# Optimization experiments

Measured on AMD Instinct MI355X. Metric: run time of the kernel, lower is better.

## Reference

```python
import jax, jax.numpy as jnp
import numpy as np

NUM_PATCHES = 4
PATCH_RADIUS = 0.2


def setup_inputs() -> dict:
    key = jax.random.key(0)
    points = jax.random.normal(key, (64, 65536, 6), dtype=jnp.float32)
    return {"points": points}


def _fps(xyz, n_samples):
    """Furthest point sampling (pointnet2 convention: start at index 0).
    xyz: (B, N, 3) -> (B, n_samples) int32 indices."""
    B, N, _ = xyz.shape

    def body(carry, _):
        min_d, last_idx = carry                                   # (B,N), (B,)
        last = jnp.take_along_axis(xyz, last_idx[:, None, None], axis=1)  # (B,1,3)
        d = jnp.sum((xyz - last) ** 2, axis=-1)                   # (B,N)
        min_d = jnp.minimum(min_d, d)
        nxt = jnp.argmax(min_d, axis=1).astype(jnp.int32)
        return (min_d, nxt), last_idx

    init = (jnp.full((B, N), 1e10, dtype=xyz.dtype),
            jnp.zeros((B,), dtype=jnp.int32))
    (_, _), idxs = jax.lax.scan(body, init, None, length=n_samples)
    return idxs.T                                                  # (B, n_samples)


def reference(points):
    B, N, C = points.shape
    xyz = points[..., :3]

    # 1) pick patch centers via FPS
    centers_idx = _fps(xyz, NUM_PATCHES)                           # (B,P)
    centers = jnp.take_along_axis(xyz, centers_idx[..., None], axis=1)  # (B,P,3)

    # 2) distance of every point to nearest center -> drop mask
    dist = jnp.linalg.norm(xyz[:, :, None, :] - centers[:, None, :, :], axis=-1)  # (B,N,P)
    min_dist = jnp.min(dist, axis=2)                               # (B,N)
    keep = min_dist >= PATCH_RADIUS                                # (B,N) bool, True = kept

    # 3) stable compaction: kept points first (original order preserved),
    #    then repeat-fill pattern valid_points[j % num_valid]
    order = jnp.argsort(jnp.logical_not(keep).astype(jnp.int32), axis=1, stable=True)  # (B,N)
    num_valid = jnp.sum(keep, axis=1)                              # (B,)
    j = jnp.arange(N, dtype=jnp.int32)[None, :]                    # (1,N)
    k = j % jnp.maximum(num_valid, 1)[:, None]                     # (B,N)
    src = jnp.take_along_axis(order, k, axis=1)                    # (B,N)
    out = jnp.take_along_axis(points, src[..., None], axis=1)      # (B,N,C)

    # all points dropped -> zeros (matches torch branch)
    return jnp.where((num_valid > 0)[:, None, None], out, jnp.zeros_like(out))
```

## Files before the change

kernel.cpp:

```cpp
#include <hip/hip_runtime.h>
#include <stdint.h>

#define NN 65536
#define BB 64
#define TPB 256
#define BLKS_PER_B 16
#define GRID (BB * BLKS_PER_B)
#define PPB 4096
#define LPT 16

__device__ __forceinline__ float sqdist(float x, float y, float z,
                                        float cx, float cy, float cz) {
    float dx = __fsub_rn(x, cx);
    float dy = __fsub_rn(y, cy);
    float dz = __fsub_rn(z, cz);
    return __fadd_rn(__fadd_rn(__fmul_rn(dx, dx), __fmul_rn(dy, dy)),
                     __fmul_rn(dz, dz));
}

__device__ __forceinline__ unsigned long long pack_key(float v, int i) {
    return ((unsigned long long)__float_as_uint(v) << 32) |
           (unsigned long long)(0xFFFFFFFFu - (unsigned)i);
}

template<int NC>
__global__ __launch_bounds__(TPB) void fps_pass(
        const float* __restrict__ pts, unsigned long long* best) {
    const int gb = blockIdx.x;
    const int b = gb >> 4, blk = gb & 15;
    const int tid = threadIdx.x;
    const int lane = tid & 63, wid = tid >> 6;
    const float* base = pts + (size_t)b * NN * 6;

    float cx[NC], cy[NC], cz[NC];
    cx[0] = base[0]; cy[0] = base[1]; cz[0] = base[2];
    #pragma unroll
    for (int k = 1; k < NC; ++k) {
        unsigned long long key = best[(k - 1) * BB + b];
        int idx = (int)(0xFFFFFFFFu - (unsigned)(key & 0xFFFFFFFFu));
        const float* p = base + (size_t)idx * 6;
        cx[k] = p[0]; cy[k] = p[1]; cz[k] = p[2];
    }

    float bestv = -1.0f; int besti = 0x7fffffff;
    #pragma unroll
    for (int l = 0; l < LPT; ++l) {
        const int p = blk * PPB + l * TPB + tid;
        const float* q = base + (size_t)p * 6;
        float2 xy = *(const float2*)q;
        float  zz = q[2];
        float d = sqdist(xy.x, xy.y, zz, cx[0], cy[0], cz[0]);
        #pragma unroll
        for (int k = 1; k < NC; ++k)
            d = fminf(d, sqdist(xy.x, xy.y, zz, cx[k], cy[k], cz[k]));
        if (d > bestv) { bestv = d; besti = p; }
    }
    unsigned long long key = pack_key(bestv, besti);
    #pragma unroll
    for (int off = 32; off > 0; off >>= 1) {
        unsigned long long ok = __shfl_down(key, off, 64);
        if (ok > key) key = ok;
    }
    __shared__ unsigned long long s_k[4];
    if (lane == 0) s_k[wid] = key;
    __syncthreads();
    if (tid == 0) {
        unsigned long long bk = s_k[0];
        #pragma unroll
        for (int w = 1; w < 4; ++w) bk = (s_k[w] > bk) ? s_k[w] : bk;
        atomicMax(&best[(NC - 1) * BB + b], bk);
    }
}

__global__ __launch_bounds__(TPB) void fps_final(
        const float* __restrict__ pts, const unsigned long long* __restrict__ best,
        uint64_t* __restrict__ masks) {
    const int gb = blockIdx.x;
    const int b = gb >> 4, blk = gb & 15;
    const int tid = threadIdx.x;
    const int lane = tid & 63, wid = tid >> 6;
    const float* base = pts + (size_t)b * NN * 6;

    float cx[4], cy[4], cz[4];
    cx[0] = base[0]; cy[0] = base[1]; cz[0] = base[2];
    #pragma unroll
    for (int k = 1; k < 4; ++k) {
        unsigned long long key = best[(k - 1) * BB + b];
        int idx = (int)(0xFFFFFFFFu - (unsigned)(key & 0xFFFFFFFFu));
        const float* p = base + (size_t)idx * 6;
        cx[k] = p[0]; cy[k] = p[1]; cz[k] = p[2];
    }
    uint64_t* mb = masks + (size_t)b * 1024;

    #pragma unroll
    for (int l = 0; l < LPT; ++l) {
        const int p = blk * PPB + l * TPB + tid;
        const float* q = base + (size_t)p * 6;
        float2 xy = *(const float2*)q;
        float  zz = q[2];
        float d = sqdist(xy.x, xy.y, zz, cx[0], cy[0], cz[0]);
        #pragma unroll
        for (int k = 1; k < 4; ++k)
            d = fminf(d, sqdist(xy.x, xy.y, zz, cx[k], cy[k], cz[k]));
        int keep = (__fsqrt_rn(d) >= 0.2f) ? 1 : 0;
        uint64_t m = __ballot(keep);
        if (lane == 0) mb[blk * 64 + l * 4 + wid] = m;
    }
}

__global__ __launch_bounds__(TPB) void compact_kernel(
        const uint64_t* __restrict__ masks, int* __restrict__ valid,
        int* __restrict__ numvalid) {
    const int b = blockIdx.x;
    const int tid = threadIdx.x;
    const int lane = tid & 63, wid = tid >> 6;
    const uint64_t* mb = masks + (size_t)b * 1024;
    uint64_t w0 = mb[tid * 4 + 0], w1 = mb[tid * 4 + 1];
    uint64_t w2 = mb[tid * 4 + 2], w3 = mb[tid * 4 + 3];
    int cnt4 = __popcll(w0) + __popcll(w1) + __popcll(w2) + __popcll(w3);
    int incl = cnt4;
    #pragma unroll
    for (int off = 1; off < 64; off <<= 1) {
        int v = __shfl_up(incl, off, 64);
        if (lane >= off) incl += v;
    }
    __shared__ int s_ws[4], s_wo[4];
    if (lane == 63) s_ws[wid] = incl;
    __syncthreads();
    if (tid == 0) {
        int run = 0;
        #pragma unroll
        for (int w = 0; w < 4; ++w) { s_wo[w] = run; run += s_ws[w]; }
        numvalid[b] = run;
    }
    __syncthreads();
    int pos = s_wo[wid] + incl - cnt4;
    int* vb = valid + ((size_t)b << 16);
    const int pbase = tid * 256;
    uint64_t ws[4] = { w0, w1, w2, w3 };
    #pragma unroll
    for (int wdx = 0; wdx < 4; ++wdx) {
        uint64_t m = ws[wdx];
        int pb = pbase + wdx * 64;
        while (m) {
            int k = __builtin_ctzll(m);
            m &= m - 1;
            vb[pos++] = pb + k;
        }
    }
}

__global__ __launch_bounds__(256) void gather_kernel(
        const float* __restrict__ pts, const int* __restrict__ valid,
        const int* __restrict__ numvalid, float* __restrict__ out) {
    const int idx = blockIdx.x * 256 + threadIdx.x;
    const int b = idx >> 16;
    const int j = idx & (NN - 1);
    const int nv = numvalid[b];
    float2* o = (float2*)(out + (size_t)idx * 6);
    if (nv <= 0) {
        float2 z = make_float2(0.f, 0.f);
        o[0] = z; o[1] = z; o[2] = z;
        return;
    }
    unsigned jj = (unsigned)j % (unsigned)nv;
    int src = valid[((size_t)b << 16) + jj];
    const float2* p = (const float2*)(pts + ((size_t)(b << 16) + (size_t)src) * 6);
    o[0] = p[0]; o[1] = p[1]; o[2] = p[2];
}

extern "C" void kernel_launch(void* const* d_in, const int* in_sizes, int n_in,
                              void* d_out, int out_size, void* d_ws, size_t ws_size,
                              hipStream_t stream) {
    const float* pts = (const float*)d_in[0];
    float* out = (float*)d_out;

    unsigned long long* best = (unsigned long long*)d_ws;
    int*      numvalid = (int*)((char*)d_ws + (4 << 10));
    uint64_t* masks    = (uint64_t*)((char*)d_ws + (64 << 10));
    int*      valid    = (int*)((char*)d_ws + (1 << 20));

    hipMemsetAsync(best, 0, 3 * BB * sizeof(unsigned long long), stream);

    fps_pass<1><<<GRID, TPB, 0, stream>>>(pts, best);
    fps_pass<2><<<GRID, TPB, 0, stream>>>(pts, best);
    fps_pass<3><<<GRID, TPB, 0, stream>>>(pts, best);
    fps_final<<<GRID, TPB, 0, stream>>>(pts, best, masks);
    compact_kernel<<<BB, TPB, 0, stream>>>(masks, valid, numvalid);
    gather_kernel<<<(BB * NN) / 256, 256, 0, stream>>>(pts, valid, numvalid, out);
}
```

Baseline: 278.3 us.

## Fuse compaction into gather and replace atomics with per-block partial keys

Removes the separate compaction kernel and its index array by having each gather block rebuild the per-batch prefix of mask popcounts in shared memory. Each output point then finds its source with a binary search plus an in-word select. The FPS passes now write per-block partial max keys, which each consumer reduces, replacing the memset and atomicMax. The FPS grid doubles to 32 blocks per batch with fewer points per thread. The cost is redundant prefix work in every gather block and a 32-way key reduction repeated per block.

```diff
diff --git a/kernel.cpp b/kernel.cpp
--- a/kernel.cpp
+++ b/kernel.cpp
@@ -4,10 +4,15 @@
 #define NN 65536
 #define BB 64
 #define TPB 256
-#define BLKS_PER_B 16
-#define GRID (BB * BLKS_PER_B)
-#define PPB 4096
-#define LPT 16
+
+#define FBPB 32
+#define FGRID (BB * FBPB)
+#define FPPB 2048
+#define FLPT 8
+
+#define GBPB 16
+#define GGRID (BB * GBPB)
+#define GLPT 16
 
 __device__ __forceinline__ float sqdist(float x, float y, float z,
                                         float cx, float cy, float cz) {
@@ -23,150 +28,192 @@
            (unsigned long long)(0xFFFFFFFFu - (unsigned)i);
 }
 
+__device__ __forceinline__ int key_idx(unsigned long long key) {
+    return (int)(0xFFFFFFFFu - (unsigned)(key & 0xFFFFFFFFu));
+}
+
+__device__ __forceinline__ int reduce_part(const unsigned long long* partKey,
+                                           int a, int b) {
+    const unsigned long long* s = partKey + a * FGRID + b * FBPB;
+    unsigned long long bk = s[0];
+    #pragma unroll
+    for (int w = 1; w < FBPB; ++w) bk = (s[w] > bk) ? s[w] : bk;
+    return key_idx(bk);
+}
+
 template<int NC>
 __global__ __launch_bounds__(TPB) void fps_pass(
-        const float* __restrict__ pts, unsigned long long* best) {
+        const float* __restrict__ pts, unsigned long long* partKey) {
+    const int gb = blockIdx.x;
+    const int b = gb >> 5, blk = gb & 31;
+    const int tid = threadIdx.x;
+    const int lane = tid & 63, wid = tid >> 6;
+    const float* base = pts + (size_t)b * NN * 6;
+
+    float cx[NC], cy[NC], cz[NC];
+    cx[0] = base[0]; cy[0] = base[1]; cz[0] = base[2];
+    #pragma unroll
+    for (int k = 1; k < NC; ++k) {
+        int idx = reduce_part(partKey, k - 1, b);
+        const float* p = base + (size_t)idx * 6;
+        cx[k] = p[0]; cy[k] = p[1]; cz[k] = p[2];
+    }
+
+    float bestv = -1.0f; int besti = 0x7fffffff;
+    #pragma unroll
+    for (int l = 0; l < FLPT; ++l) {
+        const int p = blk * FPPB + l * TPB + tid;
+        const float* q = base + (size_t)p * 6;
+        float2 xy = *(const float2*)q;
+        float  zz = q[2];
+        float d = sqdist(xy.x, xy.y, zz, cx[0], cy[0], cz[0]);
+        #pragma unroll
+        for (int k = 1; k < NC; ++k)
+            d = fminf(d, sqdist(xy.x, xy.y, zz, cx[k], cy[k], cz[k]));
+        if (d > bestv) { bestv = d; besti = p; }
+    }
+    unsigned long long key = pack_key(bestv, besti);
+    #pragma unroll
+    for (int off = 32; off > 0; off >>= 1) {
+        unsigned long long ok = __shfl_down(key, off, 64);
+        if (ok > key) key = ok;
+    }
+    __shared__ unsigned long long s_k[4];
+    if (lane == 0) s_k[wid] = key;
+    __syncthreads();
+    if (tid == 0) {
+        unsigned long long bk = s_k[0];
+        #pragma unroll
+        for (int w = 1; w < 4; ++w) bk = (s_k[w] > bk) ? s_k[w] : bk;
+        partKey[(NC - 1) * FGRID + gb] = bk;
+    }
+}
+
+__global__ __launch_bounds__(TPB) void fps_final(
+        const float* __restrict__ pts,
+        const unsigned long long* __restrict__ partKey,
+        uint64_t* __restrict__ masks) {
+    const int gb = blockIdx.x;
+    const int b = gb >> 5, blk = gb & 31;
+    const int tid = threadIdx.x;
+    const int lane = tid & 63, wid = tid >> 6;
+    const float* base = pts + (size_t)b * NN * 6;
+
+    float cx[4], cy[4], cz[4];
+    cx[0] = base[0]; cy[0] = base[1]; cz[0] = base[2];
+    #pragma unroll
+    for (int k = 1; k < 4; ++k) {
+        int idx = reduce_part(partKey, k - 1, b);
+        const float* p = base + (size_t)idx * 6;
+        cx[k] = p[0]; cy[k] = p[1]; cz[k] = p[2];
+    }
+    uint64_t* mb = masks + (size_t)b * 1024;
+
+    #pragma unroll
+    for (int l = 0; l < FLPT; ++l) {
+        const int p = blk * FPPB + l * TPB + tid;
+        const float* q = base + (size_t)p * 6;
+        float2 xy = *(const float2*)q;
+        float  zz = q[2];
+        float d = sqdist(xy.x, xy.y, zz, cx[0], cy[0], cz[0]);
+        #pragma unroll
+        for (int k = 1; k < 4; ++k)
+            d = fminf(d, sqdist(xy.x, xy.y, zz, cx[k], cy[k], cz[k]));
+        int keep = (__fsqrt_rn(d) >= 0.2f) ? 1 : 0;
+        uint64_t m = __ballot(keep);
+        if (lane == 0) mb[blk * 32 + l * 4 + wid] = m;
+    }
+}
+
+__global__ __launch_bounds__(TPB) void gather_kernel(
+        const float* __restrict__ pts, const uint64_t* __restrict__ masks,
+        float* __restrict__ out) {
     const int gb = blockIdx.x;
     const int b = gb >> 4, blk = gb & 15;
     const int tid = threadIdx.x;
     const int lane = tid & 63, wid = tid >> 6;
-    const float* base = pts + (size_t)b * NN * 6;
-
-    float cx[NC], cy[NC], cz[NC];
-    cx[0] = base[0]; cy[0] = base[1]; cz[0] = base[2];
-    #pragma unroll
-    for (int k = 1; k < NC; ++k) {
-        unsigned long long key = best[(k - 1) * BB + b];
-        int idx = (int)(0xFFFFFFFFu - (unsigned)(key & 0xFFFFFFFFu));
-        const float* p = base + (size_t)idx * 6;
-        cx[k] = p[0]; cy[k] = p[1]; cz[k] = p[2];
-    }
-
-    float bestv = -1.0f; int besti = 0x7fffffff;
-    #pragma unroll
-    for (int l = 0; l < LPT; ++l) {
-        const int p = blk * PPB + l * TPB + tid;
-        const float* q = base + (size_t)p * 6;
-        float2 xy = *(const float2*)q;
-        float  zz = q[2];
-        float d = sqdist(xy.x, xy.y, zz, cx[0], cy[0], cz[0]);
-        #pragma unroll
-        for (int k = 1; k < NC; ++k)
-            d = fminf(d, sqdist(xy.x, xy.y, zz, cx[k], cy[k], cz[k]));
-        if (d > bestv) { bestv = d; besti = p; }
-    }
-    unsigned long long key = pack_key(bestv, besti);
-    #pragma unroll
-    for (int off = 32; off > 0; off >>= 1) {
-        unsigned long long ok = __shfl_down(key, off, 64);
-        if (ok > key) key = ok;
-    }
-    __shared__ unsigned long long s_k[4];
-    if (lane == 0) s_k[wid] = key;
-    __syncthreads();
-    if (tid == 0) {
-        unsigned long long bk = s_k[0];
-        #pragma unroll
-        for (int w = 1; w < 4; ++w) bk = (s_k[w] > bk) ? s_k[w] : bk;
-        atomicMax(&best[(NC - 1) * BB + b], bk);
-    }
-}
-
-__global__ __launch_bounds__(TPB) void fps_final(
-        const float* __restrict__ pts, const unsigned long long* __restrict__ best,
-        uint64_t* __restrict__ masks) {
-    const int gb = blockIdx.x;
-    const int b = gb >> 4, blk = gb & 15;
-    const int tid = threadIdx.x;
-    const int lane = tid & 63, wid = tid >> 6;
-    const float* base = pts + (size_t)b * NN * 6;
-
-    float cx[4], cy[4], cz[4];
-    cx[0] = base[0]; cy[0] = base[1]; cz[0] = base[2];
-    #pragma unroll
-    for (int k = 1; k < 4; ++k) {
-        unsigned long long key = best[(k - 1) * BB + b];
-        int idx = (int)(0xFFFFFFFFu - (unsigned)(key & 0xFFFFFFFFu));
-        const float* p = base + (size_t)idx * 6;
-        cx[k] = p[0]; cy[k] = p[1]; cz[k] = p[2];
-    }
-    uint64_t* mb = masks + (size_t)b * 1024;
-
-    #pragma unroll
-    for (int l = 0; l < LPT; ++l) {
-        const int p = blk * PPB + l * TPB + tid;
-        const float* q = base + (size_t)p * 6;
-        float2 xy = *(const float2*)q;
-        float  zz = q[2];
-        float d = sqdist(xy.x, xy.y, zz, cx[0], cy[0], cz[0]);
-        #pragma unroll
-        for (int k = 1; k < 4; ++k)
-            d = fminf(d, sqdist(xy.x, xy.y, zz, cx[k], cy[k], cz[k]));
-        int keep = (__fsqrt_rn(d) >= 0.2f) ? 1 : 0;
-        uint64_t m = __ballot(keep);
-        if (lane == 0) mb[blk * 64 + l * 4 + wid] = m;
-    }
-}
-
-__global__ __launch_bounds__(TPB) void compact_kernel(
-        const uint64_t* __restrict__ masks, int* __restrict__ valid,
-        int* __restrict__ numvalid) {
-    const int b = blockIdx.x;
-    const int tid = threadIdx.x;
-    const int lane = tid & 63, wid = tid >> 6;
+    __shared__ uint64_t s_m[1024];
+    __shared__ int s_pre[1024];
+    __shared__ int s_ws[4], s_wo[4];
+    __shared__ int s_nv;
+
     const uint64_t* mb = masks + (size_t)b * 1024;
-    uint64_t w0 = mb[tid * 4 + 0], w1 = mb[tid * 4 + 1];
-    uint64_t w2 = mb[tid * 4 + 2], w3 = mb[tid * 4 + 3];
-    int cnt4 = __popcll(w0) + __popcll(w1) + __popcll(w2) + __popcll(w3);
-    int incl = cnt4;
+    uint64_t w[4];
+    int cnt = 0;
+    #pragma unroll
+    for (int k = 0; k < 4; ++k) {
+        w[k] = mb[tid * 4 + k];
+        s_m[tid * 4 + k] = w[k];
+        cnt += __popcll(w[k]);
+    }
+    int incl = cnt;
     #pragma unroll
     for (int off = 1; off < 64; off <<= 1) {
         int v = __shfl_up(incl, off, 64);
         if (lane >= off) incl += v;
     }
-    __shared__ int s_ws[4], s_wo[4];
     if (lane == 63) s_ws[wid] = incl;
     __syncthreads();
     if (tid == 0) {
         int run = 0;
         #pragma unroll
-        for (int w = 0; w < 4; ++w) { s_wo[w] = run; run += s_ws[w]; }
-        numvalid[b] = run;
-    }
-    __syncthreads();
-    int pos = s_wo[wid] + incl - cnt4;
-    int* vb = valid + ((size_t)b << 16);
-    const int pbase = tid * 256;
-    uint64_t ws[4] = { w0, w1, w2, w3 };
-    #pragma unroll
-    for (int wdx = 0; wdx < 4; ++wdx) {
-        uint64_t m = ws[wdx];
-        int pb = pbase + wdx * 64;
-        while (m) {
-            int k = __builtin_ctzll(m);
-            m &= m - 1;
-            vb[pos++] = pb + k;
+        for (int q = 0; q < 4; ++q) { s_wo[q] = run; run += s_ws[q]; }
+        s_nv = run;
+    }
+    __syncthreads();
+    int run = s_wo[wid] + incl - cnt;
+    #pragma unroll
+    for (int k = 0; k < 4; ++k) {
+        s_pre[tid * 4 + k] = run;
+        run += __popcll(w[k]);
+    }
+    __syncthreads();
+
+    const int nv = s_nv;
+    const float* baseP = pts + (size_t)b * NN * 6;
+    float* ob = out + (size_t)b * NN * 6;
+
+    if (nv <= 0) {
+        float2 zz = make_float2(0.f, 0.f);
+        #pragma unroll
+        for (int l = 0; l < GLPT; ++l) {
+            int j = blk * 4096 + l * TPB + tid;
+            float2* o = (float2*)(ob + (size_t)j * 6);
+            o[0] = zz; o[1] = zz; o[2] = zz;
         }
-    }
-}
-
-__global__ __launch_bounds__(256) void gather_kernel(
-        const float* __restrict__ pts, const int* __restrict__ valid,
-        const int* __restrict__ numvalid, float* __restrict__ out) {
-    const int idx = blockIdx.x * 256 + threadIdx.x;
-    const int b = idx >> 16;
-    const int j = idx & (NN - 1);
-    const int nv = numvalid[b];
-    float2* o = (float2*)(out + (size_t)idx * 6);
-    if (nv <= 0) {
-        float2 z = make_float2(0.f, 0.f);
-        o[0] = z; o[1] = z; o[2] = z;
         return;
     }
-    unsigned jj = (unsigned)j % (unsigned)nv;
-    int src = valid[((size_t)b << 16) + jj];
-    const float2* p = (const float2*)(pts + ((size_t)(b << 16) + (size_t)src) * 6);
-    o[0] = p[0]; o[1] = p[1]; o[2] = p[2];
+
+    #pragma unroll
+    for (int l = 0; l < GLPT; ++l) {
+        int j = blk * 4096 + l * TPB + tid;
+        int jj = (int)((unsigned)j % (unsigned)nv);
+        int wd = 0;
+        #pragma unroll
+        for (int s = 512; s > 0; s >>= 1) {
+            int cand = wd + s;
+            if (cand < 1024 && s_pre[cand] <= jj) wd = cand;
+        }
+        int r = jj - s_pre[wd];
+        uint64_t m = s_m[wd];
+        int bit = 0;
+        int c = __popcll(m & 0xFFFFFFFFull);
+        if (r >= c) { r -= c; m >>= 32; bit += 32; }
+        c = __popcll(m & 0xFFFFull);
+        if (r >= c) { r -= c; m >>= 16; bit += 16; }
+        c = __popcll(m & 0xFFull);
+        if (r >= c) { r -= c; m >>= 8; bit += 8; }
+        c = __popcll(m & 0xFull);
+        if (r >= c) { r -= c; m >>= 4; bit += 4; }
+        c = __popcll(m & 0x3ull);
+        if (r >= c) { r -= c; m >>= 2; bit += 2; }
+        if (r >= (int)(m & 1ull)) { bit += 1; }
+        int src = wd * 64 + bit;
+        const float2* p = (const float2*)(baseP + (size_t)src * 6);
+        float2* o = (float2*)(ob + (size_t)j * 6);
+        float2 r0 = p[0], r1 = p[1], r2 = p[2];
+        o[0] = r0; o[1] = r1; o[2] = r2;
+    }
 }
 
 extern "C" void kernel_launch(void* const* d_in, const int* in_sizes, int n_in,
@@ -175,17 +222,12 @@
     const float* pts = (const float*)d_in[0];
     float* out = (float*)d_out;
 
-    unsigned long long* best = (unsigned long long*)d_ws;
-    int*      numvalid = (int*)((char*)d_ws + (4 << 10));
-    uint64_t* masks    = (uint64_t*)((char*)d_ws + (64 << 10));
-    int*      valid    = (int*)((char*)d_ws + (1 << 20));
-
-    hipMemsetAsync(best, 0, 3 * BB * sizeof(unsigned long long), stream);
-
-    fps_pass<1><<<GRID, TPB, 0, stream>>>(pts, best);
-    fps_pass<2><<<GRID, TPB, 0, stream>>>(pts, best);
-    fps_pass<3><<<GRID, TPB, 0, stream>>>(pts, best);
-    fps_final<<<GRID, TPB, 0, stream>>>(pts, best, masks);
-    compact_kernel<<<BB, TPB, 0, stream>>>(masks, valid, numvalid);
-    gather_kernel<<<(BB * NN) / 256, 256, 0, stream>>>(pts, valid, numvalid, out);
-}
+    unsigned long long* partKey = (unsigned long long*)d_ws;
+    uint64_t* masks = (uint64_t*)((char*)d_ws + (64 << 10));
+
+    fps_pass<1><<<FGRID, TPB, 0, stream>>>(pts, partKey);
+    fps_pass<2><<<FGRID, TPB, 0, stream>>>(pts, partKey);
+    fps_pass<3><<<FGRID, TPB, 0, stream>>>(pts, partKey);
+    fps_final<<<FGRID, TPB, 0, stream>>>(pts, partKey, masks);
+    gather_kernel<<<GGRID, TPB, 0, stream>>>(pts, masks, out);
+}
```

Result: faster. 247.0 us (-11.3%).
